# Kernel optimization log

Hardware: AMD Instinct MI355X
Metric: run time of the kernel (lower is better)

## Reference

```python
import jax, jax.numpy as jnp
import numpy as np

B, S, D, F, E = 2, 1024, 1024, 4096, 8

def setup_inputs() -> dict:
    key = jax.random.key(0)
    ks = jax.random.split(key, 6)
    sc = 0.02  # typical init scale
    return {
        "sequences": jax.random.normal(ks[0], (B, S, D), jnp.float32),
        "router_w1": jax.random.normal(ks[1], (D, D), jnp.float32) * sc,
        "router_b1": jnp.zeros((D,), jnp.float32),
        "router_w2": jax.random.normal(ks[2], (D, E), jnp.float32) * sc,
        "router_b2": jnp.zeros((E,), jnp.float32),
        "expert_w1": jax.random.normal(ks[3], (E, D, F), jnp.float32) * sc,
        "expert_b1": jnp.zeros((E, F), jnp.float32),
        "expert_w2": jax.random.normal(ks[4], (E, F, D), jnp.float32) * sc,
        "expert_b2": jnp.zeros((E, D), jnp.float32),
    }

def reference(sequences, router_w1, router_b1, router_w2, router_b2,
              expert_w1, expert_b1, expert_w2, expert_b2):
    # Router: Linear -> ReLU -> Linear -> Softmax, per-token argmax expert pick
    h = jax.nn.relu(sequences @ router_w1 + router_b1)          # [B,S,D]
    probs = jax.nn.softmax(h @ router_w2 + router_b2, axis=-1)  # [B,S,E]
    idx = jnp.argmax(probs, axis=-1)                            # [B,S] int
    onehot = jax.nn.one_hot(idx, expert_w1.shape[0], dtype=sequences.dtype)  # [B,S,E]
    # Dense all-expert FFN (2-layer position-wise FC w/ ReLU, dropout=0 eval),
    # then combine with the one-hot selection (hard top-1 dispatch semantics).
    hid = jax.nn.relu(jnp.einsum('bsd,edf->ebsf', sequences, expert_w1)
                      + expert_b1[:, None, None, :])            # [E,B,S,F]
    y = jnp.einsum('ebsf,efd->ebsd', hid, expert_w2) + expert_b2[:, None, None, :]
    return jnp.einsum('ebsd,bse->bsd', y, onehot)               # [B,S,D]
```

## Files before the change

kernel.cpp:

```cpp
#include <hip/hip_runtime.h>
#include <hip/hip_bf16.h>

#define T_TOK 2048
#define DD 1024
#define FF 4096
#define EE 8

typedef __attribute__((ext_vector_type(8))) short short8;
typedef __attribute__((ext_vector_type(4))) short short4v;
typedef __attribute__((ext_vector_type(4))) float floatx4;

static __device__ __forceinline__ unsigned f2bf_u(float f){
  unsigned u = __float_as_uint(f);
  unsigned r = u + 0x7fffu + ((u >> 16) & 1u);
  return r >> 16;
}

static __device__ __forceinline__ short8 ldfrag(const unsigned short* p){
  short4v lo = *(const short4v*)p;
  short4v hi = *(const short4v*)(p + 4);
  return __builtin_shufflevector(lo, hi, 0, 1, 2, 3, 4, 5, 6, 7);
}

__global__ __launch_bounds__(256) void router_gemm1(
    const float* __restrict__ X, const float* __restrict__ W,
    const float* __restrict__ bias, float* __restrict__ H, int* counts)
{
  if (blockIdx.x == 0 && blockIdx.y == 0 && threadIdx.x < EE) counts[threadIdx.x] = 0;
  __shared__ float As[2][16][68];
  __shared__ float Bs[2][16][68];
  const int tid = threadIdx.x;
  const int tx = tid & 15, ty = tid >> 4;
  const int bm = blockIdx.y * 64, bn = blockIdx.x * 64;
  const int ar = tid >> 2, ak = (tid & 3) * 4;
  const int bk = tid >> 4, bn0 = (tid & 15) * 4;
  const float* aP = X + (size_t)(bm + ar) * DD;
  float acc[4][4] = {};
  float4 pa, pb;

  pa = *(const float4*)(aP + ak);
  pb = *(const float4*)(W + (size_t)bk * DD + bn + bn0);
  As[0][ak+0][ar] = pa.x; As[0][ak+1][ar] = pa.y;
  As[0][ak+2][ar] = pa.z; As[0][ak+3][ar] = pa.w;
  *(float4*)&Bs[0][bk][bn0] = pb;
  __syncthreads();

  for (int it = 0; it < DD/16; ++it){
    if (it + 1 < DD/16){
      const int kt = (it + 1) * 16;
      pa = *(const float4*)(aP + kt + ak);
      pb = *(const float4*)(W + (size_t)(kt + bk) * DD + bn + bn0);
    }
    const int buf = it & 1;
    #pragma unroll
    for (int k = 0; k < 16; ++k){
      float4 av = *(const float4*)&As[buf][k][ty*4];
      float4 bv = *(const float4*)&Bs[buf][k][tx*4];
      float am[4] = {av.x, av.y, av.z, av.w};
      float bm4[4] = {bv.x, bv.y, bv.z, bv.w};
      #pragma unroll
      for (int i = 0; i < 4; ++i)
        #pragma unroll
        for (int j = 0; j < 4; ++j)
          acc[i][j] += am[i] * bm4[j];
    }
    if (it + 1 < DD/16){
      const int nb2 = (it + 1) & 1;
      As[nb2][ak+0][ar] = pa.x; As[nb2][ak+1][ar] = pa.y;
      As[nb2][ak+2][ar] = pa.z; As[nb2][ak+3][ar] = pa.w;
      *(float4*)&Bs[nb2][bk][bn0] = pb;
      __syncthreads();
    }
  }
  #pragma unroll
  for (int i = 0; i < 4; ++i){
    float4 v;
    v.x = fmaxf(acc[i][0] + bias[bn + tx*4 + 0], 0.f);
    v.y = fmaxf(acc[i][1] + bias[bn + tx*4 + 1], 0.f);
    v.z = fmaxf(acc[i][2] + bias[bn + tx*4 + 2], 0.f);
    v.w = fmaxf(acc[i][3] + bias[bn + tx*4 + 3], 0.f);
    *(float4*)(H + (size_t)(bm + ty*4 + i) * DD + bn + tx*4) = v;
  }
}

__global__ __launch_bounds__(64) void router_logits_argmax(
    const float* __restrict__ H, const float* __restrict__ W2,
    const float* __restrict__ b2, int* __restrict__ eidx, int* __restrict__ counts)
{
  const int t = blockIdx.x;
  const int lane = threadIdx.x;
  const float* h = H + (size_t)t * DD;
  float acc[8] = {0,0,0,0,0,0,0,0};
  for (int d = lane; d < DD; d += 64){
    float hv = h[d];
    float4 w0 = *(const float4*)(W2 + (size_t)d * 8);
    float4 w1 = *(const float4*)(W2 + (size_t)d * 8 + 4);
    acc[0] += hv * w0.x; acc[1] += hv * w0.y; acc[2] += hv * w0.z; acc[3] += hv * w0.w;
    acc[4] += hv * w1.x; acc[5] += hv * w1.y; acc[6] += hv * w1.z; acc[7] += hv * w1.w;
  }
  #pragma unroll
  for (int s = 32; s > 0; s >>= 1)
    #pragma unroll
    for (int e2 = 0; e2 < 8; ++e2)
      acc[e2] += __shfl_down(acc[e2], s, 64);
  if (lane == 0){
    int best = 0; float bv = acc[0] + b2[0];
    #pragma unroll
    for (int e2 = 1; e2 < 8; ++e2){
      float v = acc[e2] + b2[e2];
      if (v > bv){ bv = v; best = e2; }
    }
    eidx[t] = best;
    atomicAdd(&counts[best], 1);
  }
}

__global__ void scan_offsets(const int* __restrict__ counts, int* __restrict__ offsets,
                             int* __restrict__ cursors)
{
  if (threadIdx.x == 0 && blockIdx.x == 0){
    int s = 0;
    for (int e = 0; e < EE; ++e){ offsets[e] = s; cursors[e] = s; s += counts[e]; }
    offsets[EE] = s;
  }
}

__global__ __launch_bounds__(256) void scatter_tokens(
    const int* __restrict__ eidx, int* __restrict__ cursors, int* __restrict__ perm)
{
  int t = blockIdx.x * 256 + threadIdx.x;
  if (t < T_TOK){
    int e = eidx[t];
    int p = atomicAdd(&cursors[e], 1);
    perm[p] = t;
  }
}

template<bool FIRST>
__global__ __launch_bounds__(256) void expert_gemm(
    const float* __restrict__ X,
    const unsigned short* __restrict__ hidIn,
    const float* __restrict__ Wall,
    const float* __restrict__ Ball,
    unsigned short* __restrict__ hidOut,
    float* __restrict__ Yout,
    const int* __restrict__ perm,
    const int* __restrict__ offsets)
{
  constexpr int K = FIRST ? DD : FF;
  constexpr int N = FIRST ? FF : DD;
  constexpr int NIT = K / 64;
  const int e   = blockIdx.z;
  const int off = offsets[e];
  const int cnt = offsets[e+1] - off;
  const int m0  = blockIdx.y * 64;
  if (m0 >= cnt) return;
  const int nb = blockIdx.x * 64;
  const float* W    = Wall + (size_t)e * K * N;
  const float* bias = Ball + (size_t)e * N;

  __shared__ unsigned short As[2][64 * 68];
  __shared__ unsigned short Bs[2][64 * 68];

  const int tid = threadIdx.x;
  const int ar = tid >> 2;
  const int ak = (tid & 3) * 16;
  int mrow = m0 + ar; if (mrow >= cnt) mrow = cnt - 1;
  const float* aF = nullptr;
  const unsigned short* aH = nullptr;
  if constexpr (FIRST) aF = X + (size_t)perm[off + mrow] * DD;
  else                 aH = hidIn + (size_t)(off + mrow) * FF;
  const int bkp = (tid >> 3) * 2;
  const int bn0 = (tid & 7) * 8;

  const int lane = tid & 63;
  const int w    = tid >> 6;
  const int wm   = (w & 1) * 32;
  const int wn   = (w >> 1) * 32;
  const int lrow = lane & 15;
  const int lq   = lane >> 4;

  floatx4 acc[2][2];
  #pragma unroll
  for (int i = 0; i < 2; ++i)
    #pragma unroll
    for (int j = 0; j < 2; ++j)
      acc[i][j] = (floatx4){0.f, 0.f, 0.f, 0.f};

  float4 fa[4]; uint4 ha[2];
  float4 fb[4];

  auto issue = [&](int kt){
    if constexpr (FIRST){
      #pragma unroll
      for (int i = 0; i < 4; ++i) fa[i] = *(const float4*)(aF + kt + ak + i*4);
    } else {
      ha[0] = *(const uint4*)(aH + kt + ak);
      ha[1] = *(const uint4*)(aH + kt + ak + 8);
    }
    const float* r0 = W + (size_t)(kt + bkp) * N + nb + bn0;
    fb[0] = *(const float4*)(r0);
    fb[1] = *(const float4*)(r0 + 4);
    fb[2] = *(const float4*)(r0 + N);
    fb[3] = *(const float4*)(r0 + N + 4);
  };

  auto stage = [&](int buf){
    unsigned short* a = &As[buf][ar*68 + ak];
    if constexpr (FIRST){
      #pragma unroll
      for (int i = 0; i < 4; ++i){
        const float* f = (const float*)&fa[i];
        uint2 p;
        p.x = f2bf_u(f[0]) | (f2bf_u(f[1]) << 16);
        p.y = f2bf_u(f[2]) | (f2bf_u(f[3]) << 16);
        *(uint2*)(a + i*4) = p;
      }
    } else {
      *(uint2*)(a + 0)  = make_uint2(ha[0].x, ha[0].y);
      *(uint2*)(a + 4)  = make_uint2(ha[0].z, ha[0].w);
      *(uint2*)(a + 8)  = make_uint2(ha[1].x, ha[1].y);
      *(uint2*)(a + 12) = make_uint2(ha[1].z, ha[1].w);
    }
    const float* l0 = (const float*)&fb[0];
    const float* l1 = (const float*)&fb[1];
    const float* h0 = (const float*)&fb[2];
    const float* h1 = (const float*)&fb[3];
    #pragma unroll
    for (int j = 0; j < 4; ++j){
      *(unsigned*)(&Bs[buf][(bn0 + j)*68 + bkp])     = f2bf_u(l0[j]) | (f2bf_u(h0[j]) << 16);
      *(unsigned*)(&Bs[buf][(bn0 + 4 + j)*68 + bkp]) = f2bf_u(l1[j]) | (f2bf_u(h1[j]) << 16);
    }
  };

  auto compute = [&](int buf){
    #pragma unroll
    for (int ks = 0; ks < 2; ++ks){
      short8 afr[2], bfr[2];
      #pragma unroll
      for (int i = 0; i < 2; ++i)
        afr[i] = ldfrag(&As[buf][(wm + i*16 + lrow)*68 + ks*32 + lq*8]);
      #pragma unroll
      for (int j = 0; j < 2; ++j)
        bfr[j] = ldfrag(&Bs[buf][(wn + j*16 + lrow)*68 + ks*32 + lq*8]);
      #pragma unroll
      for (int i = 0; i < 2; ++i)
        #pragma unroll
        for (int j = 0; j < 2; ++j)
          acc[i][j] = __builtin_amdgcn_mfma_f32_16x16x32_bf16(afr[i], bfr[j], acc[i][j], 0, 0, 0);
    }
  };

  issue(0);
  stage(0);
  __syncthreads();
  for (int it = 0; it < NIT; ++it){
    if (it + 1 < NIT) issue((it + 1) * 64);
    compute(it & 1);
    if (it + 1 < NIT){
      stage((it + 1) & 1);
      __syncthreads();
    }
  }

  #pragma unroll
  for (int i = 0; i < 2; ++i){
    #pragma unroll
    for (int j = 0; j < 2; ++j){
      const int n = nb + wn + j*16 + lrow;
      const float bv = bias[n];
      #pragma unroll
      for (int r = 0; r < 4; ++r){
        int m = m0 + wm + i*16 + lq*4 + r;
        if (m < cnt){
          float v = acc[i][j][r] + bv;
          if constexpr (FIRST){
            v = fmaxf(v, 0.f);
            hidOut[(size_t)(off + m) * FF + n] = (unsigned short)f2bf_u(v);
          } else {
            Yout[(size_t)perm[off + m] * DD + n] = v;
          }
        }
      }
    }
  }
}

extern "C" void kernel_launch(void* const* d_in, const int* in_sizes, int n_in,
                              void* d_out, int out_size, void* d_ws, size_t ws_size,
                              hipStream_t stream)
{
  const float* X   = (const float*)d_in[0];
  const float* rw1 = (const float*)d_in[1];
  const float* rb1 = (const float*)d_in[2];
  const float* rw2 = (const float*)d_in[3];
  const float* rb2 = (const float*)d_in[4];
  const float* ew1 = (const float*)d_in[5];
  const float* eb1 = (const float*)d_in[6];
  const float* ew2 = (const float*)d_in[7];
  const float* eb2 = (const float*)d_in[8];
  float* out = (float*)d_out;

  char* w = (char*)d_ws;
  float* H = (float*)w;                       w += (size_t)T_TOK * DD * sizeof(float);
  unsigned short* hid = (unsigned short*)w;   w += (size_t)T_TOK * FF * sizeof(short);
  int* eidx    = (int*)w;  w += T_TOK * sizeof(int);
  int* perm    = (int*)w;  w += T_TOK * sizeof(int);
  int* counts  = (int*)w;  w += 16 * sizeof(int);
  int* offsets = (int*)w;  w += 16 * sizeof(int);
  int* cursors = (int*)w;

  router_gemm1<<<dim3(DD/64, T_TOK/64), 256, 0, stream>>>(X, rw1, rb1, H, counts);
  router_logits_argmax<<<dim3(T_TOK), 64, 0, stream>>>(H, rw2, rb2, eidx, counts);
  scan_offsets<<<1, 64, 0, stream>>>(counts, offsets, cursors);
  scatter_tokens<<<dim3(T_TOK/256), 256, 0, stream>>>(eidx, cursors, perm);
  expert_gemm<true ><<<dim3(FF/64, T_TOK/64, EE), 256, 0, stream>>>(X, nullptr, ew1, eb1, hid, nullptr, perm, offsets);
  expert_gemm<false><<<dim3(DD/64, T_TOK/64, EE), 256, 0, stream>>>(nullptr, hid, ew2, eb2, nullptr, out, perm, offsets);
}
```

Measured before the change: 511.3 us.

## Enlarge expert GEMM M tile to 128 rows and use packed bf16 conversion

Doubles the token (M) tile of the expert GEMMs from 64 to 128, so each wave computes a 64x32 output with four A fragments per B fragment. Each weight tile, converted from fp32 to bf16 in shared memory, is then reused across twice as many tokens, roughly halving weight global traffic and conversion work. It also swaps the manual rounding for the packed __float22bfloat162_rn intrinsic, sets launch_bounds minimum blocks to 3, and adds compiler memory barriers to keep prefetch loads ahead of compute. The cost is more registers and LDS per block, fewer blocks, and more wasted padded rows for experts with few tokens.

After: 557.6 us. 9.0% more time.

```diff
diff --git a/kernel.cpp b/kernel.cpp
--- a/kernel.cpp
+++ b/kernel.cpp
@@ -14,6 +14,10 @@
   unsigned u = __float_as_uint(f);
   unsigned r = u + 0x7fffu + ((u >> 16) & 1u);
   return r >> 16;
+}
+static __device__ __forceinline__ unsigned pkbf(float x, float y){
+  __hip_bfloat162 h = __float22bfloat162_rn(float2{x, y});
+  return *(unsigned*)&h;
 }
 
 static __device__ __forceinline__ short8 ldfrag(const unsigned short* p){
@@ -51,6 +55,7 @@
       pa = *(const float4*)(aP + kt + ak);
       pb = *(const float4*)(W + (size_t)(kt + bk) * DD + bn + bn0);
     }
+    asm volatile("" ::: "memory");
     const int buf = it & 1;
     #pragma unroll
     for (int k = 0; k < 16; ++k){
@@ -137,7 +142,7 @@
 }
 
 template<bool FIRST>
-__global__ __launch_bounds__(256) void expert_gemm(
+__global__ __launch_bounds__(256, 3) void expert_gemm(
     const float* __restrict__ X,
     const unsigned short* __restrict__ hidIn,
     const float* __restrict__ Wall,
@@ -153,19 +158,19 @@
   const int e   = blockIdx.z;
   const int off = offsets[e];
   const int cnt = offsets[e+1] - off;
-  const int m0  = blockIdx.y * 64;
+  const int m0  = blockIdx.y * 128;
   if (m0 >= cnt) return;
   const int nb = blockIdx.x * 64;
   const float* W    = Wall + (size_t)e * K * N;
   const float* bias = Ball + (size_t)e * N;
 
-  __shared__ unsigned short As[2][64 * 68];
+  __shared__ unsigned short As[2][128 * 68];
   __shared__ unsigned short Bs[2][64 * 68];
 
   const int tid = threadIdx.x;
-  const int ar = tid >> 2;
-  const int ak = (tid & 3) * 16;
-  int mrow = m0 + ar; if (mrow >= cnt) mrow = cnt - 1;
+  const int sr = tid >> 1;
+  const int sk = (tid & 1) * 32;
+  int mrow = m0 + sr; if (mrow >= cnt) mrow = cnt - 1;
   const float* aF = nullptr;
   const unsigned short* aH = nullptr;
   if constexpr (FIRST) aF = X + (size_t)perm[off + mrow] * DD;
@@ -175,28 +180,28 @@
 
   const int lane = tid & 63;
   const int w    = tid >> 6;
-  const int wm   = (w & 1) * 32;
+  const int wm   = (w & 1) * 64;
   const int wn   = (w >> 1) * 32;
   const int lrow = lane & 15;
   const int lq   = lane >> 4;
 
-  floatx4 acc[2][2];
+  floatx4 acc[4][2];
   #pragma unroll
-  for (int i = 0; i < 2; ++i)
+  for (int i = 0; i < 4; ++i)
     #pragma unroll
     for (int j = 0; j < 2; ++j)
       acc[i][j] = (floatx4){0.f, 0.f, 0.f, 0.f};
 
-  float4 fa[4]; uint4 ha[2];
+  float4 fa[8]; uint4 ha[4];
   float4 fb[4];
 
   auto issue = [&](int kt){
     if constexpr (FIRST){
       #pragma unroll
-      for (int i = 0; i < 4; ++i) fa[i] = *(const float4*)(aF + kt + ak + i*4);
+      for (int i = 0; i < 8; ++i) fa[i] = *(const float4*)(aF + kt + sk + i*4);
     } else {
-      ha[0] = *(const uint4*)(aH + kt + ak);
-      ha[1] = *(const uint4*)(aH + kt + ak + 8);
+      #pragma unroll
+      for (int i = 0; i < 4; ++i) ha[i] = *(const uint4*)(aH + kt + sk + i*8);
     }
     const float* r0 = W + (size_t)(kt + bkp) * N + nb + bn0;
     fb[0] = *(const float4*)(r0);
@@ -206,21 +211,22 @@
   };
 
   auto stage = [&](int buf){
-    unsigned short* a = &As[buf][ar*68 + ak];
+    unsigned short* a = &As[buf][sr*68 + sk];
     if constexpr (FIRST){
       #pragma unroll
-      for (int i = 0; i < 4; ++i){
+      for (int i = 0; i < 8; ++i){
         const float* f = (const float*)&fa[i];
         uint2 p;
-        p.x = f2bf_u(f[0]) | (f2bf_u(f[1]) << 16);
-        p.y = f2bf_u(f[2]) | (f2bf_u(f[3]) << 16);
+        p.x = pkbf(f[0], f[1]);
+        p.y = pkbf(f[2], f[3]);
         *(uint2*)(a + i*4) = p;
       }
     } else {
-      *(uint2*)(a + 0)  = make_uint2(ha[0].x, ha[0].y);
-      *(uint2*)(a + 4)  = make_uint2(ha[0].z, ha[0].w);
-      *(uint2*)(a + 8)  = make_uint2(ha[1].x, ha[1].y);
-      *(uint2*)(a + 12) = make_uint2(ha[1].z, ha[1].w);
+      #pragma unroll
+      for (int i = 0; i < 4; ++i){
+        *(uint2*)(a + i*8)     = make_uint2(ha[i].x, ha[i].y);
+        *(uint2*)(a + i*8 + 4) = make_uint2(ha[i].z, ha[i].w);
+      }
     }
     const float* l0 = (const float*)&fb[0];
     const float* l1 = (const float*)&fb[1];
@@ -228,23 +234,23 @@
     const float* h1 = (const float*)&fb[3];
     #pragma unroll
     for (int j = 0; j < 4; ++j){
-      *(unsigned*)(&Bs[buf][(bn0 + j)*68 + bkp])     = f2bf_u(l0[j]) | (f2bf_u(h0[j]) << 16);
-      *(unsigned*)(&Bs[buf][(bn0 + 4 + j)*68 + bkp]) = f2bf_u(l1[j]) | (f2bf_u(h1[j]) << 16);
+      *(unsigned*)(&Bs[buf][(bn0 + j)*68 + bkp])     = pkbf(l0[j], h0[j]);
+      *(unsigned*)(&Bs[buf][(bn0 + 4 + j)*68 + bkp]) = pkbf(l1[j], h1[j]);
     }
   };
 
   auto compute = [&](int buf){
     #pragma unroll
     for (int ks = 0; ks < 2; ++ks){
-      short8 afr[2], bfr[2];
-      #pragma unroll
-      for (int i = 0; i < 2; ++i)
+      short8 afr[4], bfr[2];
+      #pragma unroll
+      for (int i = 0; i < 4; ++i)
         afr[i] = ldfrag(&As[buf][(wm + i*16 + lrow)*68 + ks*32 + lq*8]);
       #pragma unroll
       for (int j = 0; j < 2; ++j)
         bfr[j] = ldfrag(&Bs[buf][(wn + j*16 + lrow)*68 + ks*32 + lq*8]);
       #pragma unroll
-      for (int i = 0; i < 2; ++i)
+      for (int i = 0; i < 4; ++i)
         #pragma unroll
         for (int j = 0; j < 2; ++j)
           acc[i][j] = __builtin_amdgcn_mfma_f32_16x16x32_bf16(afr[i], bfr[j], acc[i][j], 0, 0, 0);
@@ -256,6 +262,7 @@
   __syncthreads();
   for (int it = 0; it < NIT; ++it){
     if (it + 1 < NIT) issue((it + 1) * 64);
+    asm volatile("" ::: "memory");
     compute(it & 1);
     if (it + 1 < NIT){
       stage((it + 1) & 1);
@@ -264,7 +271,7 @@
   }
 
   #pragma unroll
-  for (int i = 0; i < 2; ++i){
+  for (int i = 0; i < 4; ++i){
     #pragma unroll
     for (int j = 0; j < 2; ++j){
       const int n = nb + wn + j*16 + lrow;
@@ -314,6 +321,6 @@
   router_logits_argmax<<<dim3(T_TOK), 64, 0, stream>>>(H, rw2, rb2, eidx, counts);
   scan_offsets<<<1, 64, 0, stream>>>(counts, offsets, cursors);
   scatter_tokens<<<dim3(T_TOK/256), 256, 0, stream>>>(eidx, cursors, perm);
-  expert_gemm<true ><<<dim3(FF/64, T_TOK/64, EE), 256, 0, stream>>>(X, nullptr, ew1, eb1, hid, nullptr, perm, offsets);
-  expert_gemm<false><<<dim3(DD/64, T_TOK/64, EE), 256, 0, stream>>>(nullptr, hid, ew2, eb2, nullptr, out, perm, offsets);
-}
+  expert_gemm<true ><<<dim3(FF/64, T_TOK/128, EE), 256, 0, stream>>>(X, nullptr, ew1, eb1, hid, nullptr, perm, offsets);
+  expert_gemm<false><<<dim3(DD/64, T_TOK/128, EE), 256, 0, stream>>>(nullptr, hid, ew2, eb2, nullptr, out, perm, offsets);
+}
```
